# Kernel tuning notes

Hardware: AMD Instinct MI355X
Metric: run time of the kernel (lower is better)

Reference implementation:

```python
import jax, jax.numpy as jnp
import numpy as np

H = 10           # lstm_hidden / attn_hidden
OUT = 2          # output_size
VTH = 0.5        # args.vth (LSNN threshold, beta=0 so fixed)
DT = 1e-3
TAU_SYN_INV = 1.0 / 5e-3
TAU_MEM_INV = 1.0 / 1e-2


def _bn(x, g, b, eps=1e-5):
    # TdBatchNorm1d in ANN mode: BatchNorm1d over channel dim of (B, C, T), batch stats
    m = x.mean(axis=(0, 2), keepdims=True)
    v = x.var(axis=(0, 2), keepdims=True)
    return g[None, :, None] * (x - m) * jax.lax.rsqrt(v + eps) + b[None, :, None]


def _lin(x, W):
    # ModuleLayer(Linear): apply linear over channel dim of (B, C, T)
    return jnp.einsum('bct,hc->bht', x, W)


def setup_inputs() -> dict:
    key = jax.random.key(0)
    ks = jax.random.split(key, 12)
    B, C, T = 32, 64, 1024
    f32 = jnp.float32
    ones = jnp.ones((H,), f32)
    zeros = jnp.zeros((H,), f32)
    def n(k, shape, s=0.3):
        return jax.random.normal(k, shape, f32) * s
    return {
        'bs1': jax.random.normal(ks[0], (B, 1), f32),
        'bs2': jax.random.normal(ks[1], (B, 1), f32),
        'beeg': jax.random.normal(ks[2], (B, C, T), f32),
        'targets': jax.random.randint(ks[3], (B,), 0, 2),
        'W_ef': n(ks[4], (H, C)), 'b_ef': jnp.zeros((H,), f32),
        'g_i': ones, 'be_i': zeros,
        'Wq': n(ks[5], (H, H)), 'g_q': ones, 'be_q': zeros,
        'Wk': n(ks[6], (H, H)), 'g_k': ones, 'be_k': zeros,
        'Wv': n(ks[7], (H, H)), 'g_v': ones, 'be_v': zeros,
        'Wc': n(ks[8], (H, H)), 'g_c': ones, 'be_c': zeros,
        'W_in': n(ks[9], (H, H)), 'W_rec': n(ks[10], (H, H)),
        'W_cls': n(ks[11], (OUT, H)), 'b_cls': jnp.zeros((OUT,), f32),
    }


def _forward(beeg, W_ef, b_ef, g_i, be_i, Wq, g_q, be_q, Wk, g_k, be_k,
             Wv, g_v, be_v, Wc, g_c, be_c, W_in, W_rec, W_cls, b_cls):
    # front embedding + BNi + tanh : (B, C, T) -> (B, H, T)
    x = jnp.tanh(_bn(_lin(beeg, W_ef) + b_ef[None, :, None], g_i, be_i))
    # self-attention (need_sa, full dot_product path)
    q = jax.nn.relu(_bn(_lin(x, Wq), g_q, be_q))
    k = jax.nn.relu(_bn(_lin(x, Wk), g_k, be_k))
    v = jnp.tanh(_bn(_lin(x, Wv), g_v, be_v))
    w = jnp.einsum('bht,bhs->bts', q, k) / H              # (B, T, T)
    av = jnp.einsum('bts,bhs->bht', w, v)                  # (B, H, T)
    x = jax.nn.relu(_bn(_lin(av, Wc), g_c, be_c))
    # LSNN recurrence over time (norse-style LSNN, beta=0, b fixed at VTH)
    xs = jnp.transpose(x, (2, 0, 1))                       # (T, B, H)
    B = xs.shape[1]
    dtype = xs.dtype
    def lsnn_step(state, xt):
        z, vm, cur, b = state
        i_jump = cur + xt @ W_in.T + z @ W_rec.T
        v_dec = vm + DT * TAU_MEM_INV * (i_jump - vm)
        i_dec = i_jump * (1.0 - DT * TAU_SYN_INV)
        z_new = (v_dec > b).astype(dtype)
        v_new = (1.0 - z_new) * v_dec
        return (z_new, v_new, i_dec, b), z_new
    z0 = jnp.zeros((B, H), dtype)
    init = (z0, z0, z0, jnp.full((B, H), VTH, dtype))
    _, zs = jax.lax.scan(lsnn_step, init, xs)              # (T, B, H) spikes
    # LILinearCell classifier, stepped over time, then mean over T
    def li_step(state, zt):
        vm, cur = state
        i_new = cur * (1.0 - DT * TAU_SYN_INV) + zt @ W_cls.T + b_cls
        v_new = vm * (1.0 - DT * TAU_MEM_INV) + DT * TAU_MEM_INV * i_new
        return (v_new, i_new), v_new
    s0 = jnp.zeros((B, OUT), dtype)
    _, vs = jax.lax.scan(li_step, (s0, s0), zs)            # (T, B, 2)
    return vs.mean(axis=0)                                 # (B, 2) = sum/step


def reference(bs1, bs2, beeg, targets, W_ef, b_ef, g_i, be_i, Wq, g_q, be_q,
              Wk, g_k, be_k, Wv, g_v, be_v, Wc, g_c, be_c, W_in, W_rec,
              W_cls, b_cls):
    out = _forward(beeg, W_ef, b_ef, g_i, be_i, Wq, g_q, be_q, Wk, g_k, be_k,
                   Wv, g_v, be_v, Wc, g_c, be_c, W_in, W_rec, W_cls, b_cls)
    return out
```

## Files before the change

### kernel.cpp

```cpp
#include <hip/hip_runtime.h>
#include <math.h>


constexpr int B = 32, C = 64, T = 1024, H = 10;
constexpr int NT = 512;
constexpr int RS = 1028;

struct Params {
  const float *beeg, *W_ef, *b_ef, *g_i, *be_i, *Wq, *g_q, *be_q, *Wk, *g_k,
      *be_k, *Wv, *g_v, *be_v, *Wc, *g_c, *be_c, *W_in, *W_rec, *W_cls, *b_cls;
  int* cnt;
  double *P1, *P2, *P3;
  float* out;
};

template <int CTRL>
__device__ inline float dadd(float v) {
  int x = __builtin_amdgcn_update_dpp(0, __float_as_int(v), CTRL, 0xf, 0xf,
                                      true);
  return v + __int_as_float(x);
}
__device__ inline float wred63(float v) {
  v = dadd<0x111>(v);
  v = dadd<0x112>(v);
  v = dadd<0x114>(v);
  v = dadd<0x118>(v);
  v = dadd<0x142>(v);
  v = dadd<0x143>(v);
  return v;
}

__device__ inline void gbar(int* cnt, int phase, int tid) {
  __syncthreads();
  if (tid == 0) {
    __hip_atomic_fetch_add(&cnt[phase], 1, __ATOMIC_RELEASE,
                           __HIP_MEMORY_SCOPE_AGENT);
    while (__hip_atomic_load(&cnt[phase], __ATOMIC_RELAXED,
                             __HIP_MEMORY_SCOPE_AGENT) < B)
      __builtin_amdgcn_s_sleep(2);
  }
  __syncthreads();
}

__global__ void __launch_bounds__(NT) fused12(Params p) {
  const int b = blockIdx.x, tid = threadIdx.x;
  const int lane = tid & 63, wid = tid >> 6;
  const int t0 = tid, t1 = tid + NT;

  __shared__ __align__(16) float slab[T * 11];
  __shared__ __align__(16) float gtab[T];
  __shared__ double dred2[60 * 17 + 4];
  __shared__ double dtot[60];
  __shared__ float stM[30], stI[30], Ms[100], Nl[100];

  float* swred = slab;
  float* mpw   = slab + 512;

  {
    const float L2A = -0.15200309344504995f;
    const float L2D = -0.32192809488736235f;
    float m0 = (float)(T - t0), m1 = (float)(T - t1);
    gtab[t0] = (9.0f * (1.0f - exp2f(m0 * L2A)) -
                4.0f * (1.0f - exp2f(m0 * L2D))) * (1.0f / (float)T);
    gtab[t1] = (9.0f * (1.0f - exp2f(m1 * L2A)) -
                4.0f * (1.0f - exp2f(m1 * L2D))) * (1.0f / (float)T);
  }

  auto combine = [&](double* P, int Q2) {
    for (int id = tid; id < Q2 * 16; id += NT) {
      int ch = id >> 4, i = id & 15;
      double s = __hip_atomic_load(&P[ch * 32 + i], __ATOMIC_RELAXED,
                                   __HIP_MEMORY_SCOPE_AGENT) +
                 __hip_atomic_load(&P[ch * 32 + 16 + i], __ATOMIC_RELAXED,
                                   __HIP_MEMORY_SCOPE_AGENT);
      dred2[ch * 17 + i] = s;
    }
    __syncthreads();
    if (tid < Q2) {
      double s = 0.0;
#pragma unroll
      for (int i = 0; i < 16; ++i) s += dred2[tid * 17 + i];
      dtot[tid] = s;
    }
    __syncthreads();
  };

  float p1a[H], p1b[H];
#pragma unroll
  for (int h = 0; h < H; ++h) { p1a[h] = p.b_ef[h]; p1b[h] = p.b_ef[h]; }
  {
    const float* bp = p.beeg + (size_t)b * C * T;
#pragma unroll 8
    for (int c = 0; c < C; ++c) {
      float va = bp[(size_t)c * T + t0];
      float vb = bp[(size_t)c * T + t1];
#pragma unroll
      for (int h = 0; h < H; ++h) {
        float w = p.W_ef[h * C + c];
        p1a[h] = fmaf(va, w, p1a[h]);
        p1b[h] = fmaf(vb, w, p1b[h]);
      }
    }
  }
#pragma unroll
  for (int h = 0; h < H; ++h) {
    float r1 = wred63(p1a[h] + p1b[h]);
    float r2 = wred63(p1a[h] * p1a[h] + p1b[h] * p1b[h]);
    if (lane == 63) { swred[wid * 60 + h] = r1; swred[wid * 60 + 10 + h] = r2; }
  }
  __syncthreads();
  if (tid < 20) {
    float s = 0.f;
#pragma unroll
    for (int w = 0; w < 8; ++w) s += swred[w * 60 + tid];
    __hip_atomic_store(&p.P1[tid * 32 + b], (double)s, __ATOMIC_RELAXED,
                       __HIP_MEMORY_SCOPE_AGENT);
  }
  gbar(p.cnt, 0, tid);
  combine(p.P1, 20);
  if (tid < 10) {
    double mean = dtot[tid] * (1.0 / 32768.0);
    double var  = dtot[10 + tid] * (1.0 / 32768.0) - mean * mean;
    stM[tid] = (float)mean;
    stI[tid] = (float)(1.0 / sqrt(var + 1e-5));
  }
  __syncthreads();

  float xa[H], xb[H];
#pragma unroll
  for (int j = 0; j < H; ++j) {
    xa[j] = tanhf(p.g_i[j] * (p1a[j] - stM[j]) * stI[j] + p.be_i[j]);
    xb[j] = tanhf(p.g_i[j] * (p1b[j] - stM[j]) * stI[j] + p.be_i[j]);
  }
#pragma unroll
  for (int h = 0; h < H; ++h) {
    float qa = 0.f, qb = 0.f, ka = 0.f, kb = 0.f, va = 0.f, vb = 0.f;
#pragma unroll
    for (int j = 0; j < H; ++j) {
      float wq = p.Wq[h * H + j], wk = p.Wk[h * H + j], wv = p.Wv[h * H + j];
      qa = fmaf(xa[j], wq, qa); qb = fmaf(xb[j], wq, qb);
      ka = fmaf(xa[j], wk, ka); kb = fmaf(xb[j], wk, kb);
      va = fmaf(xa[j], wv, va); vb = fmaf(xb[j], wv, vb);
    }
    float r1 = wred63(qa + qb), r2 = wred63(qa * qa + qb * qb);
    float r3 = wred63(ka + kb), r4 = wred63(ka * ka + kb * kb);
    float r5 = wred63(va + vb), r6 = wred63(va * va + vb * vb);
    if (lane == 63) {
      swred[wid * 60 + h]      = r1; swred[wid * 60 + 30 + h] = r2;
      swred[wid * 60 + 10 + h] = r3; swred[wid * 60 + 40 + h] = r4;
      swred[wid * 60 + 20 + h] = r5; swred[wid * 60 + 50 + h] = r6;
    }
  }
  __syncthreads();
  if (tid < 60) {
    float s = 0.f;
#pragma unroll
    for (int w = 0; w < 8; ++w) s += swred[w * 60 + tid];
    __hip_atomic_store(&p.P2[tid * 32 + b], (double)s, __ATOMIC_RELAXED,
                       __HIP_MEMORY_SCOPE_AGENT);
  }
  gbar(p.cnt, 1, tid);
  combine(p.P2, 60);
  if (tid < 30) {
    double mean = dtot[tid] * (1.0 / 32768.0);
    double var  = dtot[30 + tid] * (1.0 / 32768.0) - mean * mean;
    stM[tid] = (float)mean;
    stI[tid] = (float)(1.0 / sqrt(var + 1e-5));
  }
  __syncthreads();

  {
    float kx[H], vx[H];
#pragma unroll
    for (int h = 0; h < H; ++h) {
      float ka = 0.f, va = 0.f;
#pragma unroll
      for (int j = 0; j < H; ++j) {
        ka = fmaf(xa[j], p.Wk[h * H + j], ka);
        va = fmaf(xa[j], p.Wv[h * H + j], va);
      }
      kx[h] = fmaxf(p.g_k[h] * (ka - stM[10 + h]) * stI[10 + h] + p.be_k[h], 0.f);
      vx[h] = tanhf(p.g_v[h] * (va - stM[20 + h]) * stI[20 + h] + p.be_v[h]);
    }
#pragma unroll
    for (int i = 0; i < H; ++i)
#pragma unroll
      for (int j = 0; j < H; ++j) {
        float r = wred63(kx[i] * vx[j]);
        if (lane == 63) mpw[wid * 100 + i * 10 + j] = r;
      }
  }
  {
    float kx[H], vx[H];
#pragma unroll
    for (int h = 0; h < H; ++h) {
      float kb = 0.f, vb = 0.f;
#pragma unroll
      for (int j = 0; j < H; ++j) {
        kb = fmaf(xb[j], p.Wk[h * H + j], kb);
        vb = fmaf(xb[j], p.Wv[h * H + j], vb);
      }
      kx[h] = fmaxf(p.g_k[h] * (kb - stM[10 + h]) * stI[10 + h] + p.be_k[h], 0.f);
      vx[h] = tanhf(p.g_v[h] * (vb - stM[20 + h]) * stI[20 + h] + p.be_v[h]);
    }
#pragma unroll
    for (int i = 0; i < H; ++i)
#pragma unroll
      for (int j = 0; j < H; ++j) {
        float r = wred63(kx[i] * vx[j]);
        if (lane == 63) mpw[wid * 100 + i * 10 + j] += r;
      }
  }
  __syncthreads();
  if (tid < 100) {
    float s = 0.f;
#pragma unroll
    for (int w = 0; w < 8; ++w) s += mpw[w * 100 + tid];
    Ms[tid] = s;
  }
  __syncthreads();

  if (tid < 100) {
    int i = tid / 10, h = tid % 10;
    float a = 0.f;
#pragma unroll
    for (int j = 0; j < H; ++j) a = fmaf(Ms[i * 10 + j], p.Wc[h * H + j], a);
    Nl[tid] = a * 0.1f;
  }
  __syncthreads();
  float pca[H], pcb[H];
  {
    float qv[H];
#pragma unroll
    for (int h = 0; h < H; ++h) {
      float qa = 0.f;
#pragma unroll
      for (int j = 0; j < H; ++j) qa = fmaf(xa[j], p.Wq[h * H + j], qa);
      qv[h] = fmaxf(p.g_q[h] * (qa - stM[h]) * stI[h] + p.be_q[h], 0.f);
    }
#pragma unroll
    for (int h = 0; h < H; ++h) {
      float a = 0.f;
#pragma unroll
      for (int i = 0; i < H; ++i) a = fmaf(qv[i], Nl[i * 10 + h], a);
      pca[h] = a;
    }
  }
  {
    float qv[H];
#pragma unroll
    for (int h = 0; h < H; ++h) {
      float qb = 0.f;
#pragma unroll
      for (int j = 0; j < H; ++j) qb = fmaf(xb[j], p.Wq[h * H + j], qb);
      qv[h] = fmaxf(p.g_q[h] * (qb - stM[h]) * stI[h] + p.be_q[h], 0.f);
    }
#pragma unroll
    for (int h = 0; h < H; ++h) {
      float a = 0.f;
#pragma unroll
      for (int i = 0; i < H; ++i) a = fmaf(qv[i], Nl[i * 10 + h], a);
      pcb[h] = a;
    }
  }
#pragma unroll
  for (int h = 0; h < H; ++h) {
    float r1 = wred63(pca[h] + pcb[h]);
    float r2 = wred63(pca[h] * pca[h] + pcb[h] * pcb[h]);
    if (lane == 63) { swred[wid * 60 + h] = r1; swred[wid * 60 + 10 + h] = r2; }
  }
  __syncthreads();
  if (tid < 20) {
    float s = 0.f;
#pragma unroll
    for (int w = 0; w < 8; ++w) s += swred[w * 60 + tid];
    __hip_atomic_store(&p.P3[tid * 32 + b], (double)s, __ATOMIC_RELAXED,
                       __HIP_MEMORY_SCOPE_AGENT);
  }
  gbar(p.cnt, 2, tid);
  combine(p.P3, 20);
  if (tid < 10) {
    double mean = dtot[tid] * (1.0 / 32768.0);
    double var  = dtot[10 + tid] * (1.0 / 32768.0) - mean * mean;
    stM[tid] = (float)mean;
    stI[tid] = (float)(1.0 / sqrt(var + 1e-5));
  }
  __syncthreads();

  {
    float ca[H];
#pragma unroll
    for (int j = 0; j < H; ++j)
      ca[j] = fmaxf(p.g_c[j] * (pca[j] - stM[j]) * stI[j] + p.be_c[j], 0.f);
#pragma unroll
    for (int h = 0; h < H; ++h) {
      float a = 0.f;
#pragma unroll
      for (int j = 0; j < H; ++j) a = fmaf(ca[j], p.W_in[h * H + j], a);
      slab[h * RS + t0] = a;
    }
#pragma unroll
    for (int j = 0; j < H; ++j)
      ca[j] = fmaxf(p.g_c[j] * (pcb[j] - stM[j]) * stI[j] + p.be_c[j], 0.f);
#pragma unroll
    for (int h = 0; h < H; ++h) {
      float a = 0.f;
#pragma unroll
      for (int j = 0; j < H; ++j) a = fmaf(ca[j], p.W_in[h * H + j], a);
      slab[h * RS + t1] = a;
    }
  }
  __syncthreads();

  if (tid < 64) {
    const float gtot = 4.9365234375f;

    const int slot = lane < H ? lane : 0;
    const float* row = slab + slot * RS;
    float wrf[H];
#pragma unroll
    for (int j = 0; j < H; ++j)
      wrf[j] = (lane < H) ? p.W_rec[lane * H + j] : 0.f;

    float cur = 0.f, vm = 0.f, S = 0.f;
    float zf = 0.f;

    auto step = [&](float iin, float gt) {
      float acc = cur + iin;
#pragma unroll
      for (int j = 0; j < H; ++j) {
        float zj = __int_as_float(
            __builtin_amdgcn_readlane(__float_as_int(zf), j));
        acc = fmaf(zj, wrf[j], acc);
      }
      float v_dec = fmaf(0.1f, acc - vm, vm);
      cur = 0.8f * acc;
      bool z = v_dec > 0.5f;
      vm = z ? 0.f : v_dec;
      zf = z ? 1.0f : 0.0f;
      S = fmaf(zf, gt, S);
    };

    float4 iA = *(const float4*)&row[0];
    float4 iB = *(const float4*)&row[4];
    float4 gA = *(const float4*)&gtab[0], gB = *(const float4*)&gtab[4];

    for (int t8 = 0; t8 < T - 8; t8 += 8) {
      float4 iN1 = *(const float4*)&row[t8 + 8];
      float4 iN2 = *(const float4*)&row[t8 + 12];
      float4 gN1 = *(const float4*)&gtab[t8 + 8];
      float4 gN2 = *(const float4*)&gtab[t8 + 12];
      step(iA.x, gA.x); step(iA.y, gA.y); step(iA.z, gA.z); step(iA.w, gA.w);
      step(iB.x, gB.x); step(iB.y, gB.y); step(iB.z, gB.z); step(iB.w, gB.w);
      iA = iN1; iB = iN2; gA = gN1; gB = gN2;
    }
    step(iA.x, gA.x); step(iA.y, gA.y); step(iA.z, gA.z); step(iA.w, gA.w);
    step(iB.x, gB.x); step(iB.y, gB.y); step(iB.z, gB.z); step(iB.w, gB.w);

    int li = lane < H ? lane : 0;
    float c0 = (lane < H) ? S * p.W_cls[li]     : 0.f;
    float c1 = (lane < H) ? S * p.W_cls[H + li] : 0.f;
    float r0 = wred63(c0), r1 = wred63(c1);
    if (lane == 63) {
      p.out[b * 2 + 0] = r0 + gtot * p.b_cls[0];
      p.out[b * 2 + 1] = r1 + gtot * p.b_cls[1];
    }
  }
}

extern "C" void kernel_launch(void* const* d_in, const int* in_sizes, int n_in,
                              void* d_out, int out_size, void* d_ws, size_t ws_size,
                              hipStream_t stream) {
  Params p;
  p.beeg  = (const float*)d_in[2];
  p.W_ef  = (const float*)d_in[4];
  p.b_ef  = (const float*)d_in[5];
  p.g_i   = (const float*)d_in[6];
  p.be_i  = (const float*)d_in[7];
  p.Wq    = (const float*)d_in[8];
  p.g_q   = (const float*)d_in[9];
  p.be_q  = (const float*)d_in[10];
  p.Wk    = (const float*)d_in[11];
  p.g_k   = (const float*)d_in[12];
  p.be_k  = (const float*)d_in[13];
  p.Wv    = (const float*)d_in[14];
  p.g_v   = (const float*)d_in[15];
  p.be_v  = (const float*)d_in[16];
  p.Wc    = (const float*)d_in[17];
  p.g_c   = (const float*)d_in[18];
  p.be_c  = (const float*)d_in[19];
  p.W_in  = (const float*)d_in[20];
  p.W_rec = (const float*)d_in[21];
  p.W_cls = (const float*)d_in[22];
  p.b_cls = (const float*)d_in[23];

  char* ws = (char*)d_ws;
  p.cnt = (int*)ws;
  p.P1  = (double*)(ws + 256);
  p.P2  = (double*)(ws + 256 + 5120);
  p.P3  = (double*)(ws + 256 + 5120 + 15360);
  p.out = (float*)d_out;

  (void)hipMemsetAsync(d_ws, 0, 256, stream);
  fused12<<<dim3(B), dim3(NT), 0, stream>>>(p);
}
```

Baseline: 221.7 us.

## Split each batch row across two blocks to double grid parallelism

The kernel now launches 64 blocks, two per batch element, each handling half of the time steps, instead of 32 blocks that each handled both halves. The per-batch attention matrix partials are exchanged through global memory with an extra grid barrier. The LSNN input currents are written to a global workspace behind another barrier, and only the first half-block runs the sequential recurrence. This aims to spread the front-end embedding and attention work over more CUs, at the cost of two additional grid-wide barriers and global round-trips for the recurrent-scan input.

```diff
diff --git a/kernel.cpp b/kernel.cpp
--- a/kernel.cpp
+++ b/kernel.cpp
@@ -4,13 +4,15 @@
 
 constexpr int B = 32, C = 64, T = 1024, H = 10;
 constexpr int NT = 512;
-constexpr int RS = 1028;
+constexpr int NB = 64;
 
 struct Params {
   const float *beeg, *W_ef, *b_ef, *g_i, *be_i, *Wq, *g_q, *be_q, *Wk, *g_k,
       *be_k, *Wv, *g_v, *be_v, *Wc, *g_c, *be_c, *W_in, *W_rec, *W_cls, *b_cls;
   int* cnt;
   double *P1, *P2, *P3;
+  float* PM;
+  float* Iin;
   float* out;
 };
 
@@ -36,42 +38,46 @@
     __hip_atomic_fetch_add(&cnt[phase], 1, __ATOMIC_RELEASE,
                            __HIP_MEMORY_SCOPE_AGENT);
     while (__hip_atomic_load(&cnt[phase], __ATOMIC_RELAXED,
-                             __HIP_MEMORY_SCOPE_AGENT) < B)
+                             __HIP_MEMORY_SCOPE_AGENT) < NB)
       __builtin_amdgcn_s_sleep(2);
   }
   __syncthreads();
 }
 
-__global__ void __launch_bounds__(NT) fused12(Params p) {
-  const int b = blockIdx.x, tid = threadIdx.x;
+__global__ void __launch_bounds__(NT) fused13(Params p) {
+  const int blk = blockIdx.x;
+  const int b = blk >> 1, half = blk & 1;
+  const int tid = threadIdx.x;
   const int lane = tid & 63, wid = tid >> 6;
-  const int t0 = tid, t1 = tid + NT;
-
-  __shared__ __align__(16) float slab[T * 11];
+  const int t = half * NT + tid;
+
+  __shared__ float swred[8 * 60];
+  __shared__ float mpw[8 * 100];
   __shared__ __align__(16) float gtab[T];
   __shared__ double dred2[60 * 17 + 4];
   __shared__ double dtot[60];
   __shared__ float stM[30], stI[30], Ms[100], Nl[100];
 
-  float* swred = slab;
-  float* mpw   = slab + 512;
-
   {
     const float L2A = -0.15200309344504995f;
     const float L2D = -0.32192809488736235f;
-    float m0 = (float)(T - t0), m1 = (float)(T - t1);
-    gtab[t0] = (9.0f * (1.0f - exp2f(m0 * L2A)) -
-                4.0f * (1.0f - exp2f(m0 * L2D))) * (1.0f / (float)T);
-    gtab[t1] = (9.0f * (1.0f - exp2f(m1 * L2A)) -
-                4.0f * (1.0f - exp2f(m1 * L2D))) * (1.0f / (float)T);
+    float m0 = (float)(T - tid), m1 = (float)(T - (tid + NT));
+    gtab[tid] = (9.0f * (1.0f - exp2f(m0 * L2A)) -
+                 4.0f * (1.0f - exp2f(m0 * L2D))) * (1.0f / (float)T);
+    gtab[tid + NT] = (9.0f * (1.0f - exp2f(m1 * L2A)) -
+                      4.0f * (1.0f - exp2f(m1 * L2D))) * (1.0f / (float)T);
   }
 
   auto combine = [&](double* P, int Q2) {
     for (int id = tid; id < Q2 * 16; id += NT) {
       int ch = id >> 4, i = id & 15;
-      double s = __hip_atomic_load(&P[ch * 32 + i], __ATOMIC_RELAXED,
+      double s = __hip_atomic_load(&P[ch * 64 + i], __ATOMIC_RELAXED,
                                    __HIP_MEMORY_SCOPE_AGENT) +
-                 __hip_atomic_load(&P[ch * 32 + 16 + i], __ATOMIC_RELAXED,
+                 __hip_atomic_load(&P[ch * 64 + 16 + i], __ATOMIC_RELAXED,
+                                   __HIP_MEMORY_SCOPE_AGENT) +
+                 __hip_atomic_load(&P[ch * 64 + 32 + i], __ATOMIC_RELAXED,
+                                   __HIP_MEMORY_SCOPE_AGENT) +
+                 __hip_atomic_load(&P[ch * 64 + 48 + i], __ATOMIC_RELAXED,
                                    __HIP_MEMORY_SCOPE_AGENT);
       dred2[ch * 17 + i] = s;
     }
@@ -85,27 +91,23 @@
     __syncthreads();
   };
 
-  float p1a[H], p1b[H];
-#pragma unroll
-  for (int h = 0; h < H; ++h) { p1a[h] = p.b_ef[h]; p1b[h] = p.b_ef[h]; }
+  float p1[H];
+#pragma unroll
+  for (int h = 0; h < H; ++h) p1[h] = p.b_ef[h];
   {
     const float* bp = p.beeg + (size_t)b * C * T;
 #pragma unroll 8
     for (int c = 0; c < C; ++c) {
-      float va = bp[(size_t)c * T + t0];
-      float vb = bp[(size_t)c * T + t1];
-#pragma unroll
-      for (int h = 0; h < H; ++h) {
-        float w = p.W_ef[h * C + c];
-        p1a[h] = fmaf(va, w, p1a[h]);
-        p1b[h] = fmaf(vb, w, p1b[h]);
-      }
+      float v = bp[(size_t)c * T + t];
+#pragma unroll
+      for (int h = 0; h < H; ++h)
+        p1[h] = fmaf(v, p.W_ef[h * C + c], p1[h]);
     }
   }
 #pragma unroll
   for (int h = 0; h < H; ++h) {
-    float r1 = wred63(p1a[h] + p1b[h]);
-    float r2 = wred63(p1a[h] * p1a[h] + p1b[h] * p1b[h]);
+    float r1 = wred63(p1[h]);
+    float r2 = wred63(p1[h] * p1[h]);
     if (lane == 63) { swred[wid * 60 + h] = r1; swred[wid * 60 + 10 + h] = r2; }
   }
   __syncthreads();
@@ -113,7 +115,7 @@
     float s = 0.f;
 #pragma unroll
     for (int w = 0; w < 8; ++w) s += swred[w * 60 + tid];
-    __hip_atomic_store(&p.P1[tid * 32 + b], (double)s, __ATOMIC_RELAXED,
+    __hip_atomic_store(&p.P1[tid * 64 + blk], (double)s, __ATOMIC_RELAXED,
                        __HIP_MEMORY_SCOPE_AGENT);
   }
   gbar(p.cnt, 0, tid);
@@ -126,25 +128,22 @@
   }
   __syncthreads();
 
-  float xa[H], xb[H];
-#pragma unroll
-  for (int j = 0; j < H; ++j) {
-    xa[j] = tanhf(p.g_i[j] * (p1a[j] - stM[j]) * stI[j] + p.be_i[j]);
-    xb[j] = tanhf(p.g_i[j] * (p1b[j] - stM[j]) * stI[j] + p.be_i[j]);
-  }
+  float xa[H];
+#pragma unroll
+  for (int j = 0; j < H; ++j)
+    xa[j] = tanhf(p.g_i[j] * (p1[j] - stM[j]) * stI[j] + p.be_i[j]);
 #pragma unroll
   for (int h = 0; h < H; ++h) {
-    float qa = 0.f, qb = 0.f, ka = 0.f, kb = 0.f, va = 0.f, vb = 0.f;
+    float qa = 0.f, ka = 0.f, va = 0.f;
 #pragma unroll
     for (int j = 0; j < H; ++j) {
-      float wq = p.Wq[h * H + j], wk = p.Wk[h * H + j], wv = p.Wv[h * H + j];
-      qa = fmaf(xa[j], wq, qa); qb = fmaf(xb[j], wq, qb);
-      ka = fmaf(xa[j], wk, ka); kb = fmaf(xb[j], wk, kb);
-      va = fmaf(xa[j], wv, va); vb = fmaf(xb[j], wv, vb);
-    }
-    float r1 = wred63(qa + qb), r2 = wred63(qa * qa + qb * qb);
-    float r3 = wred63(ka + kb), r4 = wred63(ka * ka + kb * kb);
-    float r5 = wred63(va + vb), r6 = wred63(va * va + vb * vb);
+      qa = fmaf(xa[j], p.Wq[h * H + j], qa);
+      ka = fmaf(xa[j], p.Wk[h * H + j], ka);
+      va = fmaf(xa[j], p.Wv[h * H + j], va);
+    }
+    float r1 = wred63(qa), r2 = wred63(qa * qa);
+    float r3 = wred63(ka), r4 = wred63(ka * ka);
+    float r5 = wred63(va), r6 = wred63(va * va);
     if (lane == 63) {
       swred[wid * 60 + h]      = r1; swred[wid * 60 + 30 + h] = r2;
       swred[wid * 60 + 10 + h] = r3; swred[wid * 60 + 40 + h] = r4;
@@ -156,7 +155,7 @@
     float s = 0.f;
 #pragma unroll
     for (int w = 0; w < 8; ++w) s += swred[w * 60 + tid];
-    __hip_atomic_store(&p.P2[tid * 32 + b], (double)s, __ATOMIC_RELAXED,
+    __hip_atomic_store(&p.P2[tid * 64 + blk], (double)s, __ATOMIC_RELAXED,
                        __HIP_MEMORY_SCOPE_AGENT);
   }
   gbar(p.cnt, 1, tid);
@@ -190,32 +189,20 @@
         if (lane == 63) mpw[wid * 100 + i * 10 + j] = r;
       }
   }
-  {
-    float kx[H], vx[H];
-#pragma unroll
-    for (int h = 0; h < H; ++h) {
-      float kb = 0.f, vb = 0.f;
-#pragma unroll
-      for (int j = 0; j < H; ++j) {
-        kb = fmaf(xb[j], p.Wk[h * H + j], kb);
-        vb = fmaf(xb[j], p.Wv[h * H + j], vb);
-      }
-      kx[h] = fmaxf(p.g_k[h] * (kb - stM[10 + h]) * stI[10 + h] + p.be_k[h], 0.f);
-      vx[h] = tanhf(p.g_v[h] * (vb - stM[20 + h]) * stI[20 + h] + p.be_v[h]);
-    }
-#pragma unroll
-    for (int i = 0; i < H; ++i)
-#pragma unroll
-      for (int j = 0; j < H; ++j) {
-        float r = wred63(kx[i] * vx[j]);
-        if (lane == 63) mpw[wid * 100 + i * 10 + j] += r;
-      }
-  }
   __syncthreads();
   if (tid < 100) {
     float s = 0.f;
 #pragma unroll
     for (int w = 0; w < 8; ++w) s += mpw[w * 100 + tid];
+    __hip_atomic_store(&p.PM[tid * 64 + blk], s, __ATOMIC_RELAXED,
+                       __HIP_MEMORY_SCOPE_AGENT);
+  }
+  gbar(p.cnt, 2, tid);
+  if (tid < 100) {
+    float s = __hip_atomic_load(&p.PM[tid * 64 + 2 * b], __ATOMIC_RELAXED,
+                                __HIP_MEMORY_SCOPE_AGENT) +
+              __hip_atomic_load(&p.PM[tid * 64 + 2 * b + 1], __ATOMIC_RELAXED,
+                                __HIP_MEMORY_SCOPE_AGENT);
     Ms[tid] = s;
   }
   __syncthreads();
@@ -228,7 +215,7 @@
     Nl[tid] = a * 0.1f;
   }
   __syncthreads();
-  float pca[H], pcb[H];
+  float pca[H];
   {
     float qv[H];
 #pragma unroll
@@ -246,27 +233,10 @@
       pca[h] = a;
     }
   }
-  {
-    float qv[H];
-#pragma unroll
-    for (int h = 0; h < H; ++h) {
-      float qb = 0.f;
-#pragma unroll
-      for (int j = 0; j < H; ++j) qb = fmaf(xb[j], p.Wq[h * H + j], qb);
-      qv[h] = fmaxf(p.g_q[h] * (qb - stM[h]) * stI[h] + p.be_q[h], 0.f);
-    }
-#pragma unroll
-    for (int h = 0; h < H; ++h) {
-      float a = 0.f;
-#pragma unroll
-      for (int i = 0; i < H; ++i) a = fmaf(qv[i], Nl[i * 10 + h], a);
-      pcb[h] = a;
-    }
-  }
 #pragma unroll
   for (int h = 0; h < H; ++h) {
-    float r1 = wred63(pca[h] + pcb[h]);
-    float r2 = wred63(pca[h] * pca[h] + pcb[h] * pcb[h]);
+    float r1 = wred63(pca[h]);
+    float r2 = wred63(pca[h] * pca[h]);
     if (lane == 63) { swred[wid * 60 + h] = r1; swred[wid * 60 + 10 + h] = r2; }
   }
   __syncthreads();
@@ -274,10 +244,10 @@
     float s = 0.f;
 #pragma unroll
     for (int w = 0; w < 8; ++w) s += swred[w * 60 + tid];
-    __hip_atomic_store(&p.P3[tid * 32 + b], (double)s, __ATOMIC_RELAXED,
+    __hip_atomic_store(&p.P3[tid * 64 + blk], (double)s, __ATOMIC_RELAXED,
                        __HIP_MEMORY_SCOPE_AGENT);
   }
-  gbar(p.cnt, 2, tid);
+  gbar(p.cnt, 3, tid);
   combine(p.P3, 20);
   if (tid < 10) {
     double mean = dtot[tid] * (1.0 / 32768.0);
@@ -297,26 +267,17 @@
       float a = 0.f;
 #pragma unroll
       for (int j = 0; j < H; ++j) a = fmaf(ca[j], p.W_in[h * H + j], a);
-      slab[h * RS + t0] = a;
-    }
-#pragma unroll
-    for (int j = 0; j < H; ++j)
-      ca[j] = fmaxf(p.g_c[j] * (pcb[j] - stM[j]) * stI[j] + p.be_c[j], 0.f);
-#pragma unroll
-    for (int h = 0; h < H; ++h) {
-      float a = 0.f;
-#pragma unroll
-      for (int j = 0; j < H; ++j) a = fmaf(ca[j], p.W_in[h * H + j], a);
-      slab[h * RS + t1] = a;
-    }
-  }
-  __syncthreads();
-
-  if (tid < 64) {
+      __hip_atomic_store(&p.Iin[(size_t)b * (H * T) + h * T + t], a,
+                         __ATOMIC_RELAXED, __HIP_MEMORY_SCOPE_AGENT);
+    }
+  }
+  gbar(p.cnt, 4, tid);
+
+  if (half == 0 && tid < 64) {
     const float gtot = 4.9365234375f;
 
     const int slot = lane < H ? lane : 0;
-    const float* row = slab + slot * RS;
+    const float* row = p.Iin + (size_t)b * (H * T) + (size_t)slot * T;
     float wrf[H];
 #pragma unroll
     for (int j = 0; j < H; ++j)
@@ -397,10 +358,12 @@
   char* ws = (char*)d_ws;
   p.cnt = (int*)ws;
   p.P1  = (double*)(ws + 256);
-  p.P2  = (double*)(ws + 256 + 5120);
-  p.P3  = (double*)(ws + 256 + 5120 + 15360);
+  p.P2  = (double*)(ws + 256 + 10240);
+  p.P3  = (double*)(ws + 256 + 40960);
+  p.PM  = (float*)(ws + 256 + 51200);
+  p.Iin = (float*)(ws + 77056);
   p.out = (float*)d_out;
 
   (void)hipMemsetAsync(d_ws, 0, 256, stream);
-  fused12<<<dim3(B), dim3(NT), 0, stream>>>(p);
-}
+  fused13<<<dim3(NB), dim3(NT), 0, stream>>>(p);
+}
```

Result: slower. 252.6 us (+13.9%).
